# Performance work log

Hardware: AMD Instinct MI355X
Metric: run time of the kernel (lower is better)

## Reference

```python
import jax, jax.numpy as jnp
import numpy as np

N = 100000      # nodes
E = 1600000     # edges
F_IN = 512      # num_features
HEADS = 8
C1 = 8          # per-head channels, layer 1
NCLS = 40       # num_classes
NEG_SLOPE = 0.2


def setup_inputs() -> dict:
    key = jax.random.key(0)
    ks = jax.random.split(key, 10)
    x = jax.random.normal(ks[0], (N, F_IN), jnp.float32)
    edge_index = jax.random.randint(ks[1], (2, E), 0, N, dtype=jnp.int64)
    s1 = 1.0 / np.sqrt(F_IN)
    s2 = 1.0 / np.sqrt(HEADS * C1)
    W1 = jax.random.normal(ks[2], (F_IN, HEADS * C1), jnp.float32) * s1
    att_src1 = jax.random.normal(ks[3], (HEADS, C1), jnp.float32) * s2
    att_dst1 = jax.random.normal(ks[4], (HEADS, C1), jnp.float32) * s2
    b1 = jnp.zeros((HEADS * C1,), jnp.float32)
    W2 = jax.random.normal(ks[5], (HEADS * C1, NCLS), jnp.float32) * s2
    att_src2 = jax.random.normal(ks[6], (1, NCLS), jnp.float32) * 0.1
    att_dst2 = jax.random.normal(ks[7], (1, NCLS), jnp.float32) * 0.1
    b2 = jnp.zeros((NCLS,), jnp.float32)
    return {"x": x, "edge_index": edge_index,
            "W1": W1, "att_src1": att_src1, "att_dst1": att_dst1, "b1": b1,
            "W2": W2, "att_src2": att_src2, "att_dst2": att_dst2, "b2": b2}


def gat_conv(x, src, dst, W, att_src, att_dst, b, heads, cout):
    """PyG-style GATConv (eval mode: dropout off). src->dst message flow."""
    n = x.shape[0]
    h = (x @ W).reshape(n, heads, cout)                 # [N, H, C]
    a_s = jnp.sum(h * att_src, axis=-1)                 # [N, H]
    a_d = jnp.sum(h * att_dst, axis=-1)                 # [N, H]
    e = jax.nn.leaky_relu(a_s[src] + a_d[dst], NEG_SLOPE)  # [Etot, H]
    # segment softmax over incoming edges of each dst node
    m = jax.lax.stop_gradient(jax.ops.segment_max(e, dst, num_segments=n))
    ex = jnp.exp(e - m[dst])
    den = jax.ops.segment_sum(ex, dst, num_segments=n)
    alpha = ex / (den[dst] + 1e-16)                     # [Etot, H]
    msg = h[src] * alpha[..., None]                     # [Etot, H, C]
    out = jax.ops.segment_sum(msg, dst, num_segments=n) # [N, H, C]
    return out.reshape(n, heads * cout) + b


def reference(x, edge_index, W1, att_src1, att_dst1, b1, W2, att_src2, att_dst2, b2):
    n = x.shape[0]
    loops = jnp.arange(n, dtype=edge_index.dtype)       # GATConv add_self_loops=True
    src = jnp.concatenate([edge_index[0], loops])
    dst = jnp.concatenate([edge_index[1], loops])
    h = jax.nn.elu(gat_conv(x, src, dst, W1, att_src1, att_dst1, b1, HEADS, C1))
    out = gat_conv(h, src, dst, W2, att_src2, att_dst2, b2, 1, NCLS)
    return jax.nn.log_softmax(out, axis=1)
```

## Files before the change

### kernel.cpp

```cpp
#include <hip/hip_runtime.h>
#include <hip/hip_bf16.h>
#include <math.h>

#define F_IN 512
#define HOUT 64
#define HEADS 8
#define C1 8
#define NCLS 40
#define NEG 0.2f

#define DPB 256
#define CAP 8064
#define EPT 32
#define WLD 520

typedef __attribute__((ext_vector_type(8))) short short8;
typedef __attribute__((ext_vector_type(4))) float f32x4;

__device__ __forceinline__ ushort f2b(float f) {
    union { float f; unsigned u; } v; v.f = f;
    unsigned r = (v.u + 0x7FFFu + ((v.u >> 16) & 1u)) >> 16;
    return (ushort)r;
}
__device__ __forceinline__ float b2f(ushort b) {
    union { unsigned u; float f; } v; v.u = ((unsigned)b) << 16;
    return v.f;
}
__device__ __forceinline__ float b2f_lo(unsigned u) { union { unsigned u; float f; } v; v.u = u << 16; return v.f; }
__device__ __forceinline__ float b2f_hi(unsigned u) { union { unsigned u; float f; } v; v.u = u & 0xFFFF0000u; return v.f; }


__global__ __launch_bounds__(256) void prep_k(const float* __restrict__ W1, const float* __restrict__ W2,
                                              int* __restrict__ gcur, ushort* __restrict__ Wtg,
                                              ushort* __restrict__ W2t, int nbuck) {
    int bid = blockIdx.x, t = threadIdx.x;
    if (bid < 128) {
        int idx = bid * 256 + t;
        int k = idx >> 6, c = idx & 63;
        Wtg[(size_t)c * WLD + k] = f2b(W1[idx]);
    } else if (bid < 140) {
        int idx = (bid - 128) * 256 + t;
        int c = idx >> 6, k = idx & 63;
        W2t[idx] = (c < NCLS) ? f2b(W2[k * NCLS + c]) : 0;
    } else {
        int b = (bid - 140) * 256 + t;
        if (b < nbuck) gcur[b] = b * CAP;
    }
}


__device__ void gemm1_body(int bid, const float* __restrict__ x, const ushort* __restrict__ Wtg,
                           ushort* __restrict__ h1b, int n, ushort Asd[128][40]) {
    int tid = threadIdx.x;
    int lane = tid & 63, wid = tid >> 6;
    int lr = lane & 15, lg = lane >> 4;
    int row0 = bid * 128;
    f32x4 acc[2][4];
#pragma unroll
    for (int rt = 0; rt < 2; ++rt)
#pragma unroll
        for (int ct = 0; ct < 4; ++ct) acc[rt][ct] = (f32x4){0.f, 0.f, 0.f, 0.f};

    for (int k0 = 0; k0 < F_IN; k0 += 32) {
#pragma unroll
        for (int j = 0; j < 4; ++j) {
            int idx = tid + j * 256;
            int r = idx >> 3;
            int k4 = (idx & 7) << 2;
            int gr = row0 + r;
            float4 v = (gr < n) ? *(const float4*)&x[(size_t)gr * F_IN + k0 + k4]
                                : make_float4(0.f, 0.f, 0.f, 0.f);
            ushort4 b4 = make_ushort4(f2b(v.x), f2b(v.y), f2b(v.z), f2b(v.w));
            *(ushort4*)&Asd[r][k4] = b4;
        }
        __syncthreads();
        short8 af[2], bf[4];
#pragma unroll
        for (int rt = 0; rt < 2; ++rt)
            af[rt] = *(const short8*)&Asd[wid * 32 + rt * 16 + lr][lg * 8];
#pragma unroll
        for (int ct = 0; ct < 4; ++ct)
            bf[ct] = *(const short8*)&Wtg[(size_t)(ct * 16 + lr) * WLD + k0 + lg * 8];
#pragma unroll
        for (int rt = 0; rt < 2; ++rt)
#pragma unroll
            for (int ct = 0; ct < 4; ++ct)
                acc[rt][ct] = __builtin_amdgcn_mfma_f32_16x16x32_bf16(af[rt], bf[ct], acc[rt][ct], 0, 0, 0);
        __syncthreads();
    }
#pragma unroll
    for (int rt = 0; rt < 2; ++rt)
#pragma unroll
        for (int q = 0; q < 4; ++q) {
            int gr = row0 + wid * 32 + rt * 16 + lg * 4 + q;
            if (gr < n) {
#pragma unroll
                for (int ct = 0; ct < 4; ++ct)
                    h1b[(size_t)gr * HOUT + ct * 16 + lr] = f2b(acc[rt][ct][q]);
            }
        }
}

__device__ void passA_body(int bid, const int* __restrict__ ei, int* __restrict__ gcur,
                           int* __restrict__ bkt, int E, int Etot, int nbuck,
                           int* hist, int* lbase) {
    int t = threadIdx.x;
    int base_e = bid * (256 * EPT);
    for (int j = t; j < 512; j += 256) hist[j] = 0;
    __syncthreads();
    for (int j = 0; j < EPT; ++j) {
        int idx = base_e + j * 256 + t;
        if (idx < Etot) {
            int d = (idx < E) ? ei[E + idx] : (idx - E);
            atomicAdd(&hist[d >> 8], 1);
        }
    }
    __syncthreads();
    for (int j = t; j < nbuck; j += 256) {
        int c = hist[j];
        lbase[j] = c ? atomicAdd(&gcur[j], c) : 0;
    }
    __syncthreads();
    for (int j = t; j < 512; j += 256) hist[j] = 0;
    __syncthreads();
    for (int j = 0; j < EPT; ++j) {
        int idx = base_e + j * 256 + t;
        if (idx < Etot) {
            int s, d;
            if (idx < E) { s = ei[idx]; d = ei[E + idx]; } else { s = idx - E; d = idx - E; }
            int b = d >> 8;
            int slot = atomicAdd(&hist[b], 1);
            bkt[lbase[b] + slot] = (s << 8) | (d & 255);
        }
    }
}

__global__ __launch_bounds__(256) void work1_k(const float* __restrict__ x, const ushort* __restrict__ Wtg,
                                               ushort* __restrict__ h1b, int n,
                                               const int* __restrict__ ei, int* __restrict__ gcur,
                                               int* __restrict__ bkt, int E, int Etot, int nbuck, int g1) {
    __shared__ ushort Asd[128][40];
    __shared__ int hist[512];
    __shared__ int lbase[512];
    if ((int)blockIdx.x < g1) gemm1_body(blockIdx.x, x, Wtg, h1b, n, Asd);
    else passA_body(blockIdx.x - g1, ei, gcur, bkt, E, Etot, nbuck, hist, lbase);
}


__global__ __launch_bounds__(512) void bscan_k(const int* __restrict__ gcur, int* __restrict__ bbase,
                                               int* __restrict__ rowptr, int nbuck, int n, int Etot) {
    __shared__ int wsum[8];
    int t = threadIdx.x;
    int v = (t < nbuck) ? gcur[t] - t * CAP : 0;
    int lane = t & 63, w = t >> 6;
    int ss = v;
#pragma unroll
    for (int off = 1; off < 64; off <<= 1) { int t2 = __shfl_up(ss, off); if (lane >= off) ss += t2; }
    if (lane == 63) wsum[w] = ss;
    __syncthreads();
    int woff = 0;
    for (int j = 0; j < w; ++j) woff += wsum[j];
    if (t < nbuck) bbase[t] = woff + ss - v;
    if (t == 0) rowptr[n] = Etot;
}


__device__ void passB_body(int b, const int* __restrict__ bkt, const int* __restrict__ gcur,
                           const int* __restrict__ bbase, int* __restrict__ rowptr,
                           int* __restrict__ col, int n, int* hist, int* lcur, int* wsum) {
    int t = threadIdx.x;
    int cnt = gcur[b] - b * CAP;
    int base = bbase[b];
    int d0 = b * DPB;
    int ndst = min(DPB, n - d0);
    const int* src = bkt + (size_t)b * CAP;
    hist[t] = 0;
    __syncthreads();
    for (int e = t; e < cnt; e += 256) {
        atomicAdd(&hist[src[e] & 255], 1);
    }
    __syncthreads();
    int v = hist[t];
    int lane = t & 63, w = t >> 6;
    int ss = v;
#pragma unroll
    for (int off = 1; off < 64; off <<= 1) { int t2 = __shfl_up(ss, off); if (lane >= off) ss += t2; }
    if (lane == 63) wsum[w] = ss;
    __syncthreads();
    int woff = 0;
    for (int j = 0; j < w; ++j) woff += wsum[j];
    int excl = woff + ss - v;
    if (t < ndst) rowptr[d0 + t] = base + excl;
    lcur[t] = excl;
    __syncthreads();
    for (int e = t; e < cnt; e += 256) {
        int u = src[e];
        int pos = atomicAdd(&lcur[u & 255], 1);
        col[base + pos] = (int)((unsigned)u >> 8);
    }
}

__device__ void att1_body(int bid, const ushort* __restrict__ h1b, const float* __restrict__ asw,
                          const float* __restrict__ adw, float* __restrict__ as1,
                          float* __restrict__ ad1, int n) {
    int t = bid * 256 + threadIdx.x;
    if (t >= n * HEADS) return;
    int hd = t & 7;
    const ushort* hp = h1b + (size_t)(t >> 3) * HOUT + hd * C1;
    short8 hv = *(const short8*)hp;
    float4 a0 = *(const float4*)(asw + hd * C1), a1 = *(const float4*)(asw + hd * C1 + 4);
    float4 d0 = *(const float4*)(adw + hd * C1), d1 = *(const float4*)(adw + hd * C1 + 4);
    float h0 = b2f((ushort)hv[0]), h1 = b2f((ushort)hv[1]), h2 = b2f((ushort)hv[2]), h3 = b2f((ushort)hv[3]);
    float h4 = b2f((ushort)hv[4]), h5 = b2f((ushort)hv[5]), h6 = b2f((ushort)hv[6]), h7 = b2f((ushort)hv[7]);
    as1[t] = h0*a0.x + h1*a0.y + h2*a0.z + h3*a0.w + h4*a1.x + h5*a1.y + h6*a1.z + h7*a1.w;
    ad1[t] = h0*d0.x + h1*d0.y + h2*d0.z + h3*d0.w + h4*d1.x + h5*d1.y + h6*d1.z + h7*d1.w;
}

__global__ __launch_bounds__(256) void work2_k(const int* __restrict__ bkt, const int* __restrict__ gcur,
                                               const int* __restrict__ bbase, int* __restrict__ rowptr,
                                               int* __restrict__ col, int n,
                                               const ushort* __restrict__ h1b, const float* __restrict__ asw,
                                               const float* __restrict__ adw, float* __restrict__ as1,
                                               float* __restrict__ ad1, int gpb) {
    __shared__ int hist[DPB];
    __shared__ int lcur[DPB];
    __shared__ int wsum[4];
    if ((int)blockIdx.x < gpb) passB_body(blockIdx.x, bkt, gcur, bbase, rowptr, col, n, hist, lcur, wsum);
    else att1_body(blockIdx.x - gpb, h1b, asw, adw, as1, ad1, n);
}


__global__ __launch_bounds__(256) void l1agg_k(const ushort* __restrict__ h1b, const float* __restrict__ as1,
                                               const float* __restrict__ ad1, const float* __restrict__ b1,
                                               const int* __restrict__ rowptr, const int* __restrict__ col,
                                               ushort* __restrict__ hactb, int n) {
    __shared__ int2 pk_all[4][2 * 273];
    int wid = threadIdx.x >> 6, lane = threadIdx.x & 63;
    int nA = (blockIdx.x * 4 + wid) * 2;
    if (nA >= n) return;
    int nB = nA + 1;
    int na = lane >> 5, sl = lane & 31;
    int node = nA + na;
    bool nodev = node < n;
    int r0 = rowptr[nA];
    int r1 = rowptr[nA + 1];
    int r2 = (nB < n) ? rowptr[nB + 1] : r1;
    int degA = r1 - r0, degB = r2 - r1;
    int st  = na ? r1 : r0;
    int deg = na ? degB : degA;
    int2* pk = pk_all[wid];

    if (degA <= 32 && degB <= 32) {
        bool v = nodev && (sl < deg);
        int s = 0;
        float4 a0 = make_float4(0.f, 0.f, 0.f, 0.f), a1 = a0;
        if (v) {
            s = col[st + sl];
            a0 = *(const float4*)&as1[s * 8];
            a1 = *(const float4*)&as1[s * 8 + 4];
        }
        float4 d0 = make_float4(0.f, 0.f, 0.f, 0.f), d1 = d0;
        if (nodev) {
            d0 = *(const float4*)&ad1[node * 8];
            d1 = *(const float4*)&ad1[node * 8 + 4];
        }
        float ea[8] = {a0.x + d0.x, a0.y + d0.y, a0.z + d0.z, a0.w + d0.w,
                       a1.x + d1.x, a1.y + d1.y, a1.z + d1.z, a1.w + d1.w};
#pragma unroll
        for (int h = 0; h < 8; ++h) {
            float e0 = ea[h];
            float ee = v ? (e0 >= 0.f ? e0 : NEG * e0) : -1e30f;
            pk[na * 273 + h * 34 + sl] = make_int2(__float_as_int(ee), s);
        }
        __asm__ volatile("s_waitcnt lgkmcnt(0)" ::: "memory");
        __builtin_amdgcn_sched_barrier(0);
        {
            int t = lane & 3, h = (lane >> 2) & 7, na2 = lane >> 5;
            int base = na2 * 273 + h * 34;
            float e[8];
#pragma unroll
            for (int u = 0; u < 8; ++u) e[u] = __int_as_float(pk[base + t + 4 * u].x);
            float mx = e[0];
#pragma unroll
            for (int u = 1; u < 8; ++u) mx = fmaxf(mx, e[u]);
            mx = fmaxf(mx, __shfl_xor(mx, 1));
            mx = fmaxf(mx, __shfl_xor(mx, 2));
            float p[8], sm = 0.f;
#pragma unroll
            for (int u = 0; u < 8; ++u) { p[u] = __expf(e[u] - mx); sm += p[u]; }
            sm += __shfl_xor(sm, 1);
            sm += __shfl_xor(sm, 2);
            float inv = 1.f / (sm + 1e-16f);
#pragma unroll
            for (int u = 0; u < 8; ++u) pk[base + t + 4 * u].x = __float_as_int(p[u] * inv);
        }
        __asm__ volatile("s_waitcnt lgkmcnt(0)" ::: "memory");
        __builtin_amdgcn_sched_barrier(0);
        int cl = sl & 15;
        int eo = sl >> 4;
        int pb = na * 273 + (cl >> 1) * 34 + eo;
        float acc0 = 0.f, acc1 = 0.f, acc2 = 0.f, acc3 = 0.f;
        int mdeg = max(degA, degB);
#pragma unroll 2
        for (int g = 0; 2 * g < mdeg; ++g) {
            int2 p2 = pk[pb + 2 * g];
            float w = __int_as_float(p2.x);
            uint2 hv = *(const uint2*)&h1b[(size_t)p2.y * HOUT + 4 * cl];
            acc0 += w * b2f_lo(hv.x);
            acc1 += w * b2f_hi(hv.x);
            acc2 += w * b2f_lo(hv.y);
            acc3 += w * b2f_hi(hv.y);
        }
        acc0 += __shfl_xor(acc0, 16);
        acc1 += __shfl_xor(acc1, 16);
        acc2 += __shfl_xor(acc2, 16);
        acc3 += __shfl_xor(acc3, 16);
        if (nodev && eo == 0) {
            float4 bb = *(const float4*)&b1[4 * cl];
            float o0 = acc0 + bb.x, o1 = acc1 + bb.y, o2 = acc2 + bb.z, o3 = acc3 + bb.w;
            float e0 = o0 > 0.f ? o0 : expm1f(o0);
            float e1 = o1 > 0.f ? o1 : expm1f(o1);
            float e2 = o2 > 0.f ? o2 : expm1f(o2);
            float e3 = o3 > 0.f ? o3 : expm1f(o3);
            ushort4 op = make_ushort4(f2b(e0), f2b(e1), f2b(e2), f2b(e3));
            *(ushort4*)&hactb[(size_t)node * HOUT + 4 * cl] = op;
        }
    } else {
        int hd = sl >> 2;
        float ad = nodev ? ad1[node * 8 + hd] : 0.f;
        float m = -1e30f, den = 0.f, a0 = 0.f, a1 = 0.f;
        int en = st + deg;
        for (int e = st; e < en; ++e) {
            int s = col[e];
            float e0 = as1[s * 8 + hd] + ad;
            float ee = e0 >= 0.f ? e0 : NEG * e0;
            unsigned hv = *(const unsigned*)&h1b[(size_t)s * HOUT + 2 * sl];
            float mn = fmaxf(m, ee);
            float sc = __expf(m - mn), p = __expf(ee - mn);
            den = den * sc + p;
            a0 = a0 * sc + p * b2f_lo(hv);
            a1 = a1 * sc + p * b2f_hi(hv);
            m = mn;
        }
        float2 bb = *(const float2*)&b1[2 * sl];
        float o0 = a0 / (den + 1e-16f) + bb.x;
        float o1 = a1 / (den + 1e-16f) + bb.y;
        float e0 = o0 > 0.f ? o0 : expm1f(o0);
        float e1 = o1 > 0.f ? o1 : expm1f(o1);
        unsigned op = (unsigned)f2b(e0) | ((unsigned)f2b(e1) << 16);
        if (nodev) *(unsigned*)&hactb[(size_t)node * HOUT + 2 * sl] = op;
    }
}


__global__ __launch_bounds__(256) void g2_k(const ushort* __restrict__ hactb, const ushort* __restrict__ W2t,
                                            const float* __restrict__ asw, const float* __restrict__ adw,
                                            ushort* __restrict__ h2b, float* __restrict__ as2,
                                            float* __restrict__ ad2, int n) {
    int tid = threadIdx.x;
    int lane = tid & 63, wid = tid >> 6;
    int lr = lane & 15, lg = lane >> 4;
    int row0 = blockIdx.x * 64 + wid * 16;
    if (row0 >= n) return;
    int gr = row0 + lr;
    bool vr = gr < n;
    f32x4 acc[3];
#pragma unroll
    for (int ct = 0; ct < 3; ++ct) acc[ct] = (f32x4){0.f, 0.f, 0.f, 0.f};
    const short8 z8 = (short8){0, 0, 0, 0, 0, 0, 0, 0};
#pragma unroll
    for (int ks = 0; ks < 2; ++ks) {
        short8 af = vr ? *(const short8*)&hactb[(size_t)gr * HOUT + ks * 32 + lg * 8] : z8;
#pragma unroll
        for (int ct = 0; ct < 3; ++ct) {
            short8 bf = *(const short8*)&W2t[(ct * 16 + lr) * HOUT + ks * 32 + lg * 8];
            acc[ct] = __builtin_amdgcn_mfma_f32_16x16x32_bf16(af, bf, acc[ct], 0, 0, 0);
        }
    }
    float av4[4], dv4[4];
#pragma unroll
    for (int q = 0; q < 4; ++q) {
        int r = row0 + lg * 4 + q;
        bool vw = r < n;
        float av = 0.f, dv = 0.f;
#pragma unroll
        for (int ct = 0; ct < 3; ++ct) {
            int c = ct * 16 + lr;
            if (c < NCLS) {
                float o = acc[ct][q];
                av += o * asw[c];
                dv += o * adw[c];
                if (vw) h2b[(size_t)r * NCLS + c] = f2b(o);
            }
        }
        av += __shfl_xor(av, 1); av += __shfl_xor(av, 2); av += __shfl_xor(av, 4); av += __shfl_xor(av, 8);
        dv += __shfl_xor(dv, 1); dv += __shfl_xor(dv, 2); dv += __shfl_xor(dv, 4); dv += __shfl_xor(dv, 8);
        av4[q] = av; dv4[q] = dv;
    }
#pragma unroll
    for (int q = 0; q < 4; ++q) {
        int r = row0 + lg * 4 + q;
        if (lr == q && r < n) as2[r] = av4[q];
        if (lr == 8 + q && r < n) ad2[r] = dv4[q];
    }
}


__global__ __launch_bounds__(256) void l2agg_k(const ushort* __restrict__ h2b, const float* __restrict__ as2,
                                               const float* __restrict__ ad2, const float* __restrict__ b2,
                                               const int* __restrict__ rowptr, const int* __restrict__ col,
                                               float* __restrict__ out, int n) {
    __shared__ int2 pk_all[4][2 * 40];
    int wid = threadIdx.x >> 6, lane = threadIdx.x & 63;
    int nA = (blockIdx.x * 4 + wid) * 2;
    if (nA >= n) return;
    int nB = nA + 1;
    int na = lane >> 5, sl = lane & 31;
    int node = nA + na;
    bool nodev = node < n;
    int r0 = rowptr[nA];
    int r1 = rowptr[nA + 1];
    int r2 = (nB < n) ? rowptr[nB + 1] : r1;
    int degA = r1 - r0, degB = r2 - r1;
    int st  = na ? r1 : r0;
    int deg = na ? degB : degA;

    if (degA <= 32 && degB <= 32) {
        int2* pk = pk_all[wid];
        bool v = nodev && (sl < deg);
        int s = 0; float av = 0.f;
        if (v) { s = col[st + sl]; av = as2[s]; }
        float ad = nodev ? ad2[node] : 0.f;
        float ev = av + ad;
        float ee = v ? (ev >= 0.f ? ev : NEG * ev) : -1e30f;
        float m = ee;
        m = fmaxf(m, __shfl_xor(m, 1)); m = fmaxf(m, __shfl_xor(m, 2));
        m = fmaxf(m, __shfl_xor(m, 4)); m = fmaxf(m, __shfl_xor(m, 8));
        m = fmaxf(m, __shfl_xor(m, 16));
        float p = __expf(ee - m);
        float d = p;
        d += __shfl_xor(d, 1); d += __shfl_xor(d, 2); d += __shfl_xor(d, 4);
        d += __shfl_xor(d, 8); d += __shfl_xor(d, 16);
        float w = p / (d + 1e-16f);
        pk[na * 40 + sl] = make_int2(__float_as_int(w), s);
        __asm__ volatile("s_waitcnt lgkmcnt(0)" ::: "memory");
        __builtin_amdgcn_sched_barrier(0);
        bool gact = sl < 20;
        int cl = sl % 10;
        int eo = sl / 10;
        float acc0 = 0.f, acc1 = 0.f, acc2 = 0.f, acc3 = 0.f;
        int mdeg = max(degA, degB);
#pragma unroll 2
        for (int g = 0; 2 * g < mdeg; ++g) {
            int j = gact ? (2 * g + eo) : 0;
            int2 p2 = pk[na * 40 + j];
            float wv = __int_as_float(p2.x);
            if (gact) {
                uint2 hv = *(const uint2*)&h2b[(size_t)p2.y * NCLS + 4 * cl];
                acc0 += wv * b2f_lo(hv.x);
                acc1 += wv * b2f_hi(hv.x);
                acc2 += wv * b2f_lo(hv.y);
                acc3 += wv * b2f_hi(hv.y);
            }
        }
        int self = threadIdx.x & 63;
        float p0 = __shfl(acc0, self + 10);
        float p1 = __shfl(acc1, self + 10);
        float p2s = __shfl(acc2, self + 10);
        float p3 = __shfl(acc3, self + 10);
        bool fin = sl < 10;
        float z0, z1, z2, z3;
        if (fin) {
            float4 bb = *(const float4*)&b2[4 * cl];
            z0 = acc0 + p0 + bb.x; z1 = acc1 + p1 + bb.y;
            z2 = acc2 + p2s + bb.z; z3 = acc3 + p3 + bb.w;
        } else { z0 = z1 = z2 = z3 = -1e30f; }
        float zm = fin ? fmaxf(fmaxf(z0, z1), fmaxf(z2, z3)) : -1e30f;
        zm = fmaxf(zm, __shfl_xor(zm, 1)); zm = fmaxf(zm, __shfl_xor(zm, 2));
        zm = fmaxf(zm, __shfl_xor(zm, 4)); zm = fmaxf(zm, __shfl_xor(zm, 8));
        float ex = fin ? (__expf(z0 - zm) + __expf(z1 - zm) + __expf(z2 - zm) + __expf(z3 - zm)) : 0.f;
        ex += __shfl_xor(ex, 1); ex += __shfl_xor(ex, 2);
        ex += __shfl_xor(ex, 4); ex += __shfl_xor(ex, 8);
        float ls = logf(ex);
        if (fin && nodev) {
            float4 o = make_float4(z0 - zm - ls, z1 - zm - ls, z2 - zm - ls, z3 - zm - ls);
            *(float4*)&out[(size_t)node * NCLS + 4 * cl] = o;
        }
    } else {
        bool act = sl < 20;
        float z0, z1;
        float ad = nodev ? ad2[node] : 0.f;
        float m = -1e30f, den = 0.f, a0 = 0.f, a1 = 0.f;
        int en = st + deg;
        for (int e = st; e < en; ++e) {
            int s = col[e];
            float ev = as2[s] + ad;
            float ee = ev >= 0.f ? ev : NEG * ev;
            float mn = fmaxf(m, ee);
            float sc = __expf(m - mn), p = __expf(ee - mn);
            den = den * sc + p;
            if (act) {
                unsigned hv = *(const unsigned*)&h2b[(size_t)s * NCLS + 2 * sl];
                a0 = a0 * sc + p * b2f_lo(hv);
                a1 = a1 * sc + p * b2f_hi(hv);
            }
            m = mn;
        }
        if (act) {
            float2 bb = *(const float2*)&b2[2 * sl];
            z0 = a0 / (den + 1e-16f) + bb.x;
            z1 = a1 / (den + 1e-16f) + bb.y;
        } else { z0 = z1 = -1e30f; }
        float zm = fmaxf(z0, z1);
        zm = fmaxf(zm, __shfl_xor(zm, 1)); zm = fmaxf(zm, __shfl_xor(zm, 2));
        zm = fmaxf(zm, __shfl_xor(zm, 4)); zm = fmaxf(zm, __shfl_xor(zm, 8));
        zm = fmaxf(zm, __shfl_xor(zm, 16));
        float ex = act ? (__expf(z0 - zm) + __expf(z1 - zm)) : 0.f;
        ex += __shfl_xor(ex, 1); ex += __shfl_xor(ex, 2); ex += __shfl_xor(ex, 4);
        ex += __shfl_xor(ex, 8); ex += __shfl_xor(ex, 16);
        float ls = logf(ex);
        if (act && nodev) {
            float2 o = make_float2(z0 - zm - ls, z1 - zm - ls);
            *(float2*)&out[(size_t)node * NCLS + 2 * sl] = o;
        }
    }
}


extern "C" void kernel_launch(void* const* d_in, const int* in_sizes, int n_in,
                              void* d_out, int out_size, void* d_ws, size_t ws_size,
                              hipStream_t stream) {
    const float* x    = (const float*)d_in[0];
    const int*   ei   = (const int*)d_in[1];
    const float* W1   = (const float*)d_in[2];
    const float* asw1 = (const float*)d_in[3];
    const float* adw1 = (const float*)d_in[4];
    const float* b1   = (const float*)d_in[5];
    const float* W2   = (const float*)d_in[6];
    const float* asw2 = (const float*)d_in[7];
    const float* adw2 = (const float*)d_in[8];
    const float* b2   = (const float*)d_in[9];
    float* out = (float*)d_out;

    const int n = in_sizes[0] / F_IN;
    const int E = in_sizes[1] / 2;
    const int Etot = E + n;
    const int nbuck = (n + DPB - 1) / DPB;
    const int npair = (n + 1) / 2;

    char* ws = (char*)d_ws;
    size_t off = 0;
    auto alloc = [&](size_t bytes) -> void* {
        void* p = ws + off;
        off = (off + bytes + 255) & ~(size_t)255;
        return p;
    };
    int*    gcur   = (int*)alloc((size_t)nbuck * 4);
    int*    bbase  = (int*)alloc((size_t)nbuck * 4);
    int*    rowptr = (int*)alloc((size_t)(n + 1) * 4);
    int*    col    = (int*)alloc((size_t)Etot * 4);
    int*    bkt    = (int*)alloc((size_t)nbuck * CAP * 4);
    ushort* h1b    = (ushort*)alloc((size_t)n * HOUT * 2);
    float*  as1    = (float*)alloc((size_t)n * HEADS * 4);
    float*  ad1    = (float*)alloc((size_t)n * HEADS * 4);
    ushort* hactb  = (ushort*)alloc((size_t)n * HOUT * 2);
    ushort* Wtg    = (ushort*)alloc((size_t)HOUT * WLD * 2);
    ushort* W2t    = (ushort*)alloc((size_t)48 * HOUT * 2);
    ushort* h2b = h1b;
    float*  as2 = (float*)(h1b + (size_t)n * NCLS);
    float*  ad2 = as2 + n;

    const int g1 = (n + 127) / 128;
    const int gpa = (Etot + 256 * EPT - 1) / (256 * EPT);
    const int gpb = nbuck;
    const int gat = (n * HEADS + 255) / 256;

    prep_k<<<142, 256, 0, stream>>>(W1, W2, gcur, Wtg, W2t, nbuck);
    work1_k<<<g1 + gpa, 256, 0, stream>>>(x, Wtg, h1b, n, ei, gcur, bkt, E, Etot, nbuck, g1);
    bscan_k<<<1, 512, 0, stream>>>(gcur, bbase, rowptr, nbuck, n, Etot);
    work2_k<<<gpb + gat, 256, 0, stream>>>(bkt, gcur, bbase, rowptr, col, n,
                                           h1b, asw1, adw1, as1, ad1, gpb);
    l1agg_k<<<(npair + 3) / 4, 256, 0, stream>>>(h1b, as1, ad1, b1, rowptr, col, hactb, n);
    g2_k<<<(n + 63) / 64, 256, 0, stream>>>(hactb, W2t, asw2, adw2, h2b, as2, ad2, n);
    l2agg_k<<<(npair + 3) / 4, 256, 0, stream>>>(h2b, as2, ad2, b2, rowptr, col, out, n);
}
```

Measured before the change: 233.7 us.

## Replace CSR rowptr with bucket-padded start/end pairs, drop scan kernel, unroll gathers

Removes the single-block bucket scan kernel by placing each bucket's column list at a fixed CAP-strided offset and storing per-node (start,end) pairs instead of a compact rowptr. The aggregation kernels load both nodes' ranges with one int4 load. The gather loops in both aggregation kernels are also unrolled by four to put more independent loads in flight. The cost is a larger, padded col array, and the unrolled loops read pk slots past the degree, which relies on those slots being zero-weighted.

```diff
diff --git a/kernel.cpp b/kernel.cpp
--- a/kernel.cpp
+++ b/kernel.cpp
@@ -147,30 +147,12 @@
 }
 
 
-__global__ __launch_bounds__(512) void bscan_k(const int* __restrict__ gcur, int* __restrict__ bbase,
-                                               int* __restrict__ rowptr, int nbuck, int n, int Etot) {
-    __shared__ int wsum[8];
-    int t = threadIdx.x;
-    int v = (t < nbuck) ? gcur[t] - t * CAP : 0;
-    int lane = t & 63, w = t >> 6;
-    int ss = v;
-#pragma unroll
-    for (int off = 1; off < 64; off <<= 1) { int t2 = __shfl_up(ss, off); if (lane >= off) ss += t2; }
-    if (lane == 63) wsum[w] = ss;
-    __syncthreads();
-    int woff = 0;
-    for (int j = 0; j < w; ++j) woff += wsum[j];
-    if (t < nbuck) bbase[t] = woff + ss - v;
-    if (t == 0) rowptr[n] = Etot;
-}
-
-
 __device__ void passB_body(int b, const int* __restrict__ bkt, const int* __restrict__ gcur,
-                           const int* __restrict__ bbase, int* __restrict__ rowptr,
-                           int* __restrict__ col, int n, int* hist, int* lcur, int* wsum) {
+                           int2* __restrict__ rowse, int* __restrict__ col, int n,
+                           int* hist, int* lcur, int* wsum) {
     int t = threadIdx.x;
     int cnt = gcur[b] - b * CAP;
-    int base = bbase[b];
+    int base = b * CAP;
     int d0 = b * DPB;
     int ndst = min(DPB, n - d0);
     const int* src = bkt + (size_t)b * CAP;
@@ -190,7 +172,7 @@
     int woff = 0;
     for (int j = 0; j < w; ++j) woff += wsum[j];
     int excl = woff + ss - v;
-    if (t < ndst) rowptr[d0 + t] = base + excl;
+    if (t < ndst) rowse[d0 + t] = make_int2(base + excl, base + excl + v);
     lcur[t] = excl;
     __syncthreads();
     for (int e = t; e < cnt; e += 256) {
@@ -217,22 +199,21 @@
 }
 
 __global__ __launch_bounds__(256) void work2_k(const int* __restrict__ bkt, const int* __restrict__ gcur,
-                                               const int* __restrict__ bbase, int* __restrict__ rowptr,
-                                               int* __restrict__ col, int n,
+                                               int2* __restrict__ rowse, int* __restrict__ col, int n,
                                                const ushort* __restrict__ h1b, const float* __restrict__ asw,
                                                const float* __restrict__ adw, float* __restrict__ as1,
                                                float* __restrict__ ad1, int gpb) {
     __shared__ int hist[DPB];
     __shared__ int lcur[DPB];
     __shared__ int wsum[4];
-    if ((int)blockIdx.x < gpb) passB_body(blockIdx.x, bkt, gcur, bbase, rowptr, col, n, hist, lcur, wsum);
+    if ((int)blockIdx.x < gpb) passB_body(blockIdx.x, bkt, gcur, rowse, col, n, hist, lcur, wsum);
     else att1_body(blockIdx.x - gpb, h1b, asw, adw, as1, ad1, n);
 }
 
 
 __global__ __launch_bounds__(256) void l1agg_k(const ushort* __restrict__ h1b, const float* __restrict__ as1,
                                                const float* __restrict__ ad1, const float* __restrict__ b1,
-                                               const int* __restrict__ rowptr, const int* __restrict__ col,
+                                               const int2* __restrict__ rowse, const int* __restrict__ col,
                                                ushort* __restrict__ hactb, int n) {
     __shared__ int2 pk_all[4][2 * 273];
     int wid = threadIdx.x >> 6, lane = threadIdx.x & 63;
@@ -242,11 +223,10 @@
     int na = lane >> 5, sl = lane & 31;
     int node = nA + na;
     bool nodev = node < n;
-    int r0 = rowptr[nA];
-    int r1 = rowptr[nA + 1];
-    int r2 = (nB < n) ? rowptr[nB + 1] : r1;
-    int degA = r1 - r0, degB = r2 - r1;
-    int st  = na ? r1 : r0;
+    int4 rr = *(const int4*)&rowse[nA];
+    if (nB >= n) { rr.z = rr.y; rr.w = rr.y; }
+    int degA = rr.y - rr.x, degB = rr.w - rr.z;
+    int st  = na ? rr.z : rr.x;
     int deg = na ? degB : degA;
     int2* pk = pk_all[wid];
 
@@ -301,15 +281,21 @@
         int pb = na * 273 + (cl >> 1) * 34 + eo;
         float acc0 = 0.f, acc1 = 0.f, acc2 = 0.f, acc3 = 0.f;
         int mdeg = max(degA, degB);
-#pragma unroll 2
-        for (int g = 0; 2 * g < mdeg; ++g) {
-            int2 p2 = pk[pb + 2 * g];
-            float w = __int_as_float(p2.x);
-            uint2 hv = *(const uint2*)&h1b[(size_t)p2.y * HOUT + 4 * cl];
-            acc0 += w * b2f_lo(hv.x);
-            acc1 += w * b2f_hi(hv.x);
-            acc2 += w * b2f_lo(hv.y);
-            acc3 += w * b2f_hi(hv.y);
+        for (int g0 = 0; 2 * g0 < mdeg; g0 += 4) {
+            int2 qa = pk[pb + 2 * g0];
+            int2 qb = pk[pb + 2 * g0 + 2];
+            int2 qc = pk[pb + 2 * g0 + 4];
+            int2 qd = pk[pb + 2 * g0 + 6];
+            uint2 ha = *(const uint2*)&h1b[(size_t)qa.y * HOUT + 4 * cl];
+            uint2 hb = *(const uint2*)&h1b[(size_t)qb.y * HOUT + 4 * cl];
+            uint2 hc = *(const uint2*)&h1b[(size_t)qc.y * HOUT + 4 * cl];
+            uint2 hd = *(const uint2*)&h1b[(size_t)qd.y * HOUT + 4 * cl];
+            float wa = __int_as_float(qa.x), wb = __int_as_float(qb.x);
+            float wc = __int_as_float(qc.x), wd = __int_as_float(qd.x);
+            acc0 += wa * b2f_lo(ha.x) + wb * b2f_lo(hb.x) + wc * b2f_lo(hc.x) + wd * b2f_lo(hd.x);
+            acc1 += wa * b2f_hi(ha.x) + wb * b2f_hi(hb.x) + wc * b2f_hi(hc.x) + wd * b2f_hi(hd.x);
+            acc2 += wa * b2f_lo(ha.y) + wb * b2f_lo(hb.y) + wc * b2f_lo(hc.y) + wd * b2f_lo(hd.y);
+            acc3 += wa * b2f_hi(ha.y) + wb * b2f_hi(hb.y) + wc * b2f_hi(hc.y) + wd * b2f_hi(hd.y);
         }
         acc0 += __shfl_xor(acc0, 16);
         acc1 += __shfl_xor(acc1, 16);
@@ -408,7 +394,7 @@
 
 __global__ __launch_bounds__(256) void l2agg_k(const ushort* __restrict__ h2b, const float* __restrict__ as2,
                                                const float* __restrict__ ad2, const float* __restrict__ b2,
-                                               const int* __restrict__ rowptr, const int* __restrict__ col,
+                                               const int2* __restrict__ rowse, const int* __restrict__ col,
                                                float* __restrict__ out, int n) {
     __shared__ int2 pk_all[4][2 * 40];
     int wid = threadIdx.x >> 6, lane = threadIdx.x & 63;
@@ -418,11 +404,10 @@
     int na = lane >> 5, sl = lane & 31;
     int node = nA + na;
     bool nodev = node < n;
-    int r0 = rowptr[nA];
-    int r1 = rowptr[nA + 1];
-    int r2 = (nB < n) ? rowptr[nB + 1] : r1;
-    int degA = r1 - r0, degB = r2 - r1;
-    int st  = na ? r1 : r0;
+    int4 rr = *(const int4*)&rowse[nA];
+    if (nB >= n) { rr.z = rr.y; rr.w = rr.y; }
+    int degA = rr.y - rr.x, degB = rr.w - rr.z;
+    int st  = na ? rr.z : rr.x;
     int deg = na ? degB : degA;
 
     if (degA <= 32 && degB <= 32) {
@@ -447,20 +432,26 @@
         __builtin_amdgcn_sched_barrier(0);
         bool gact = sl < 20;
         int cl = sl % 10;
-        int eo = sl / 10;
+        int eo2 = gact ? (sl / 10) : 0;
+        int jb = na * 40 + eo2;
         float acc0 = 0.f, acc1 = 0.f, acc2 = 0.f, acc3 = 0.f;
         int mdeg = max(degA, degB);
-#pragma unroll 2
-        for (int g = 0; 2 * g < mdeg; ++g) {
-            int j = gact ? (2 * g + eo) : 0;
-            int2 p2 = pk[na * 40 + j];
-            float wv = __int_as_float(p2.x);
+        for (int g0 = 0; 2 * g0 < mdeg; g0 += 4) {
+            int2 qa = pk[jb + 2 * g0];
+            int2 qb = pk[jb + 2 * g0 + 2];
+            int2 qc = pk[jb + 2 * g0 + 4];
+            int2 qd = pk[jb + 2 * g0 + 6];
             if (gact) {
-                uint2 hv = *(const uint2*)&h2b[(size_t)p2.y * NCLS + 4 * cl];
-                acc0 += wv * b2f_lo(hv.x);
-                acc1 += wv * b2f_hi(hv.x);
-                acc2 += wv * b2f_lo(hv.y);
-                acc3 += wv * b2f_hi(hv.y);
+                uint2 ha = *(const uint2*)&h2b[(size_t)qa.y * NCLS + 4 * cl];
+                uint2 hb = *(const uint2*)&h2b[(size_t)qb.y * NCLS + 4 * cl];
+                uint2 hc = *(const uint2*)&h2b[(size_t)qc.y * NCLS + 4 * cl];
+                uint2 hd = *(const uint2*)&h2b[(size_t)qd.y * NCLS + 4 * cl];
+                float wa = __int_as_float(qa.x), wb = __int_as_float(qb.x);
+                float wc = __int_as_float(qc.x), wd = __int_as_float(qd.x);
+                acc0 += wa * b2f_lo(ha.x) + wb * b2f_lo(hb.x) + wc * b2f_lo(hc.x) + wd * b2f_lo(hd.x);
+                acc1 += wa * b2f_hi(ha.x) + wb * b2f_hi(hb.x) + wc * b2f_hi(hc.x) + wd * b2f_hi(hd.x);
+                acc2 += wa * b2f_lo(ha.y) + wb * b2f_lo(hb.y) + wc * b2f_lo(hc.y) + wd * b2f_lo(hd.y);
+                acc3 += wa * b2f_hi(ha.y) + wb * b2f_hi(hb.y) + wc * b2f_hi(hc.y) + wd * b2f_hi(hd.y);
             }
         }
         int self = threadIdx.x & 63;
@@ -556,9 +547,8 @@
         return p;
     };
     int*    gcur   = (int*)alloc((size_t)nbuck * 4);
-    int*    bbase  = (int*)alloc((size_t)nbuck * 4);
-    int*    rowptr = (int*)alloc((size_t)(n + 1) * 4);
-    int*    col    = (int*)alloc((size_t)Etot * 4);
+    int2*   rowse  = (int2*)alloc((size_t)(n + 2) * 8);
+    int*    col    = (int*)alloc((size_t)nbuck * CAP * 4);
     int*    bkt    = (int*)alloc((size_t)nbuck * CAP * 4);
     ushort* h1b    = (ushort*)alloc((size_t)n * HOUT * 2);
     float*  as1    = (float*)alloc((size_t)n * HEADS * 4);
@@ -577,10 +567,9 @@
 
     prep_k<<<142, 256, 0, stream>>>(W1, W2, gcur, Wtg, W2t, nbuck);
     work1_k<<<g1 + gpa, 256, 0, stream>>>(x, Wtg, h1b, n, ei, gcur, bkt, E, Etot, nbuck, g1);
-    bscan_k<<<1, 512, 0, stream>>>(gcur, bbase, rowptr, nbuck, n, Etot);
-    work2_k<<<gpb + gat, 256, 0, stream>>>(bkt, gcur, bbase, rowptr, col, n,
+    work2_k<<<gpb + gat, 256, 0, stream>>>(bkt, gcur, rowse, col, n,
                                            h1b, asw1, adw1, as1, ad1, gpb);
-    l1agg_k<<<(npair + 3) / 4, 256, 0, stream>>>(h1b, as1, ad1, b1, rowptr, col, hactb, n);
+    l1agg_k<<<(npair + 3) / 4, 256, 0, stream>>>(h1b, as1, ad1, b1, rowse, col, hactb, n);
     g2_k<<<(n + 63) / 64, 256, 0, stream>>>(hactb, W2t, asw2, adw2, h2b, as2, ad2, n);
-    l2agg_k<<<(npair + 3) / 4, 256, 0, stream>>>(h2b, as2, ad2, b2, rowptr, col, out, n);
-}
+    l2agg_k<<<(npair + 3) / 4, 256, 0, stream>>>(h2b, as2, ad2, b2, rowse, col, out, n);
+}
```

Result: faster. 218.1 us (-6.7%).
